# Performance work log

Measured on AMD Instinct MI355X. Metric: run time of the kernel, lower is better.

Reference implementation:

```python
import jax, jax.numpy as jnp
import numpy as np

NUM_PARTS = 10
COP_W = 10.0
COP_K = 100.0
RES = 0.7874


def setup_inputs() -> dict:
    key = jax.random.key(0)
    k1, k2, k3, k4, k5, k6 = jax.random.split(key, 6)
    B, V, F, NHD = 256, 6890, 13776, 20000
    vertices = jax.random.normal(k1, (B, V, 3), dtype=jnp.float32)
    pressure = jax.random.uniform(k2, (B, 120, 40), dtype=jnp.float32)
    bw = jax.random.uniform(k3, (NHD, 3), dtype=jnp.float32)
    bary_w = bw / bw.sum(axis=1, keepdims=True)  # barycentric weights sum to 1
    faces = jax.random.randint(k4, (F, 3), 0, V, dtype=jnp.int64)
    face_sample = jax.random.randint(k5, (NHD,), 0, F, dtype=jnp.int64)
    face_part = jax.random.randint(k6, (F,), 0, NUM_PARTS, dtype=jnp.int64)
    return {"vertices": vertices, "pressure": pressure, "bary_w": bary_w,
            "faces": faces, "face_sample": face_sample, "face_part": face_part}


def cal_cop(pressure, resolution=RES):
    B, Y, X = pressure.shape
    x_coords = jnp.arange(X, dtype=pressure.dtype)
    y_coords = jnp.arange(Y, dtype=pressure.dtype)
    total = pressure.sum(axis=(1, 2))
    total = jnp.where(total == 0, jnp.asarray(1e-8, pressure.dtype), total)
    x_ws = (pressure * x_coords).sum(axis=(1, 2))
    y_ws = (pressure * y_coords[:, None]).sum(axis=(1, 2))
    x_c = x_ws / total
    y_c = y_ws / total
    cop_x = 0.01 * (x_c - 18.0) / resolution
    cop_y = 0.01 * (86.0 - y_c) / resolution
    cop_xy = jnp.stack([cop_x, cop_y, jnp.zeros_like(cop_x)], axis=1)
    cop_sensor_xy = jnp.stack([x_c, y_c], axis=1)
    return cop_xy, cop_sensor_xy


def reference(vertices, pressure, bary_w, faces, face_sample, face_part):
    # ---- per-part volume: signed tetrahedron volume per face, segment-summed per part
    tri = vertices[:, faces]                       # [B, F, 3, 3]
    v0, v1, v2 = tri[:, :, 0], tri[:, :, 1], tri[:, :, 2]
    tet = jnp.einsum('bfi,bfi->bf', v0, jnp.cross(v1, v2)) / 6.0   # [B, F]
    per_part_volume = jax.vmap(
        lambda t: jax.ops.segment_sum(t, face_part, num_segments=NUM_PARTS)
    )(tet)                                          # [B, P]

    # ---- HD mesh: barycentric sampling of 20000 points from faces
    fv = faces[face_sample]                         # [NHD, 3]
    vertices_hd = jnp.einsum('bnkc,nk->bnc', vertices[:, fv], bary_w)  # [B, NHD, 3]

    # ---- vertex-id -> part-volume mapping (one-hot sparse matmul == gather)
    vol_per_vert = per_part_volume[:, face_part[face_sample]]          # [B, NHD]

    com = (vertices_hd * vol_per_vert[..., None]).sum(axis=1) / \
          vol_per_vert.sum(axis=1, keepdims=True)                      # [B, 3]
    com_xy = jnp.stack([com[:, 0], com[:, 1], jnp.zeros_like(com[:, 0])], axis=1)
    com_mat = jnp.stack([com[:, 0] * 48.0, (59.0 / 33.0 - com[:, 1]) * 33.0], axis=1)

    cop_xy, _cop_mat = cal_cop(pressure)

    eps = 1e-6
    vh = vertices_hd[:, :, 1]                       # height above ground plane
    inside = (vh < 0.0).astype(vh.dtype)
    pw = inside * (1.0 - COP_K * vh) + (1.0 - inside) * jnp.exp(-COP_W * vh)
    cop = (vertices_hd * pw[..., None]).sum(axis=1) / (pw.sum(axis=1, keepdims=True) + eps)
    cop_mat_ipman = jnp.stack([cop[:, 0] + 18.0 / 78.74,
                               86.0 / 78.74 - cop[:, 1]], axis=1) * 100.0 * 0.7874

    stability_loss = jnp.linalg.norm(com_xy - cop_xy, axis=1).mean()
    return stability_loss, com_mat, cop_mat_ipman
```

## Files before the change

kernel.cpp:

```cpp
#include <hip/hip_runtime.h>
#include <math.h>

#define NB 256
#define NV 6890
#define NF 13776
#define NFP 16384
#define NHD 20000
#define NHDP 20480
#define NPARTS 10
#define PY 120
#define PX 40
#define THREADS 1024
#define NWAVES (THREADS / 64)

#define WS_DIST_OFF  0
#define WS_TABF_OFF  1024
#define WS_TABS_OFF  (WS_TABF_OFF + NFP * 16)
#define WS_TABW_OFF  (WS_TABS_OFF + NHDP * 16)
#define WS_NEEDED    (WS_TABW_OFF + NHDP * 16)

__device__ __forceinline__ float wred(float v) {
#pragma unroll
    for (int off = 32; off; off >>= 1) v += __shfl_down(v, off, 64);
    return v;
}

__global__ __launch_bounds__(256) void build_tabs(const int* __restrict__ faces,
                                                  const int* __restrict__ face_part,
                                                  const int* __restrict__ face_sample,
                                                  const float* __restrict__ bary_w,
                                                  int4* __restrict__ tabF,
                                                  int4* __restrict__ tabS,
                                                  float4* __restrict__ tabW) {
    const int i = blockIdx.x * 256 + threadIdx.x;
    if (i < NF)
        tabF[i] = make_int4(faces[3 * i + 0], faces[3 * i + 1], faces[3 * i + 2], face_part[i]);
    else if (i < NFP)
        tabF[i] = make_int4(0, 0, 0, 15);
    if (i < NHD) {
        const int fs = face_sample[i];
        tabS[i] = make_int4(faces[3 * fs + 0], faces[3 * fs + 1], faces[3 * fs + 2],
                            face_part[fs]);
        tabW[i] = make_float4(bary_w[3 * i + 0], bary_w[3 * i + 1], bary_w[3 * i + 2], 1.0f);
    } else if (i < NHDP) {
        tabS[i] = make_int4(0, 0, 0, 0);
        tabW[i] = make_float4(0.0f, 0.0f, 0.0f, 0.0f);
    }
}

__device__ __forceinline__ float tet_of(const float2* __restrict__ svxy,
                                        const float* __restrict__ svz, int4 q) {
    const float2 a = svxy[q.x];
    const float2 b = svxy[q.y];
    const float2 c = svxy[q.z];
    const float az = svz[q.x], bz = svz[q.y], cz = svz[q.z];
    return (a.x * (b.y * cz - bz * c.y) + a.y * (bz * c.x - b.x * cz) +
            az * (b.x * c.y - b.y * c.x)) * (1.0f / 6.0f);
}

template <bool TAB>
__global__ __launch_bounds__(THREADS, 4) void stab_main(
    const float* __restrict__ vertices,
    const float* __restrict__ pressure,
    const float* __restrict__ bary_w,
    const int*   __restrict__ faces,
    const int*   __restrict__ face_sample,
    const int*   __restrict__ face_part,
    const int4*  __restrict__ tabF,
    const int4*  __restrict__ tabS,
    const float4* __restrict__ tabW,
    float* __restrict__ out,
    float* __restrict__ dist)
{
    const int b    = blockIdx.x;
    const int tid  = threadIdx.x;
    const int wave = tid >> 6;
    const int lane = tid & 63;

    __shared__ float2 svxy[NV];
    __shared__ float  svz[NV];
    __shared__ float  red[NWAVES][12];
    __shared__ float  ppv[NPARTS];

    const float* vb = vertices + (size_t)b * (NV * 3);
    for (int v = tid; v < NV; v += THREADS) {
        svxy[v] = make_float2(vb[3 * v + 0], vb[3 * v + 1]);
        svz[v]  = vb[3 * v + 2];
    }
    __syncthreads();

    float pv[NPARTS];
#pragma unroll
    for (int p = 0; p < NPARTS; ++p) pv[p] = 0.0f;

    if constexpr (TAB) {
        for (int f0 = tid; f0 < NFP; f0 += 4 * THREADS) {
            const int4 q0 = tabF[f0];
            const int4 q1 = tabF[f0 + THREADS];
            const int4 q2 = tabF[f0 + 2 * THREADS];
            const int4 q3 = tabF[f0 + 3 * THREADS];
            const float t0 = tet_of(svxy, svz, q0);
            const float t1 = tet_of(svxy, svz, q1);
            const float t2 = tet_of(svxy, svz, q2);
            const float t3 = tet_of(svxy, svz, q3);
#pragma unroll
            for (int p = 0; p < NPARTS; ++p) {
                pv[p] += (q0.w == p) ? t0 : 0.0f;
                pv[p] += (q1.w == p) ? t1 : 0.0f;
                pv[p] += (q2.w == p) ? t2 : 0.0f;
                pv[p] += (q3.w == p) ? t3 : 0.0f;
            }
        }
    } else {
        for (int f = tid; f < NF; f += THREADS) {
            const int4 q = make_int4(faces[3 * f + 0], faces[3 * f + 1], faces[3 * f + 2],
                                     face_part[f]);
            const float t = tet_of(svxy, svz, q);
#pragma unroll
            for (int p = 0; p < NPARTS; ++p) pv[p] += (q.w == p) ? t : 0.0f;
        }
    }
#pragma unroll
    for (int p = 0; p < NPARTS; ++p) {
        const float r = wred(pv[p]);
        if (lane == 0) red[wave][p] = r;
    }
    __syncthreads();
    if (tid < NPARTS) {
        float s = 0.0f;
#pragma unroll
        for (int w = 0; w < NWAVES; ++w) s += red[w][tid];
        ppv[tid] = s;
    }
    __syncthreads();

    float cnx = 0.f, cny = 0.f, cd = 0.f;
    float pnx = 0.f, pny = 0.f, pd = 0.f;

    if constexpr (TAB) {
        for (int n0 = tid; n0 < NHDP; n0 += 4 * THREADS) {
            const int4   q0 = tabS[n0];
            const int4   q1 = tabS[n0 + THREADS];
            const int4   q2 = tabS[n0 + 2 * THREADS];
            const int4   q3 = tabS[n0 + 3 * THREADS];
            const float4 w0 = tabW[n0];
            const float4 w1 = tabW[n0 + THREADS];
            const float4 w2 = tabW[n0 + 2 * THREADS];
            const float4 w3 = tabW[n0 + 3 * THREADS];

            const float2 a0 = svxy[q0.x], b0 = svxy[q0.y], c0 = svxy[q0.z];
            const float2 a1 = svxy[q1.x], b1 = svxy[q1.y], c1 = svxy[q1.z];
            const float2 a2 = svxy[q2.x], b2 = svxy[q2.y], c2 = svxy[q2.z];
            const float2 a3 = svxy[q3.x], b3 = svxy[q3.y], c3 = svxy[q3.z];

            const float hx0 = w0.x * a0.x + w0.y * b0.x + w0.z * c0.x;
            const float hy0 = w0.x * a0.y + w0.y * b0.y + w0.z * c0.y;
            const float hx1 = w1.x * a1.x + w1.y * b1.x + w1.z * c1.x;
            const float hy1 = w1.x * a1.y + w1.y * b1.y + w1.z * c1.y;
            const float hx2 = w2.x * a2.x + w2.y * b2.x + w2.z * c2.x;
            const float hy2 = w2.x * a2.y + w2.y * b2.y + w2.z * c2.y;
            const float hx3 = w3.x * a3.x + w3.y * b3.x + w3.z * c3.x;
            const float hy3 = w3.x * a3.y + w3.y * b3.y + w3.z * c3.y;

            const float vol0 = ppv[q0.w] * w0.w;
            const float vol1 = ppv[q1.w] * w1.w;
            const float vol2 = ppv[q2.w] * w2.w;
            const float vol3 = ppv[q3.w] * w3.w;

            const float pw0 = ((hy0 < 0.0f) ? (1.0f - 100.0f * hy0) : __expf(-10.0f * hy0)) * w0.w;
            const float pw1 = ((hy1 < 0.0f) ? (1.0f - 100.0f * hy1) : __expf(-10.0f * hy1)) * w1.w;
            const float pw2 = ((hy2 < 0.0f) ? (1.0f - 100.0f * hy2) : __expf(-10.0f * hy2)) * w2.w;
            const float pw3 = ((hy3 < 0.0f) ? (1.0f - 100.0f * hy3) : __expf(-10.0f * hy3)) * w3.w;

            cnx += hx0 * vol0 + hx1 * vol1 + hx2 * vol2 + hx3 * vol3;
            cny += hy0 * vol0 + hy1 * vol1 + hy2 * vol2 + hy3 * vol3;
            cd  += vol0 + vol1 + vol2 + vol3;
            pnx += hx0 * pw0 + hx1 * pw1 + hx2 * pw2 + hx3 * pw3;
            pny += hy0 * pw0 + hy1 * pw1 + hy2 * pw2 + hy3 * pw3;
            pd  += pw0 + pw1 + pw2 + pw3;
        }
    } else {
        for (int n = tid; n < NHD; n += THREADS) {
            const int fs = face_sample[n];
            const int i0 = faces[3 * fs + 0], i1 = faces[3 * fs + 1], i2 = faces[3 * fs + 2];
            const float w0 = bary_w[3 * n + 0], w1 = bary_w[3 * n + 1], w2 = bary_w[3 * n + 2];
            const float2 a = svxy[i0], bb = svxy[i1], c = svxy[i2];
            const float hx = w0 * a.x + w1 * bb.x + w2 * c.x;
            const float hy = w0 * a.y + w1 * bb.y + w2 * c.y;
            const float vol = ppv[face_part[fs]];
            cnx += hx * vol; cny += hy * vol; cd += vol;
            const float pw = (hy < 0.0f) ? (1.0f - 100.0f * hy) : __expf(-10.0f * hy);
            pnx += hx * pw; pny += hy * pw; pd += pw;
        }
    }

    float pt = 0.f, pxs = 0.f, pys = 0.f;
    const float4* pb4 = (const float4*)(pressure + (size_t)b * (PY * PX));
    for (int i = tid; i < (PY * PX) / 4; i += THREADS) {
        const float4 v = pb4[i];
        const int idx = 4 * i;
        const float xb = (float)(idx % PX);
        const float yb = (float)(idx / PX);
        const float srow = v.x + v.y + v.z + v.w;
        pt  += srow;
        pxs += v.x * xb + v.y * (xb + 1.0f) + v.z * (xb + 2.0f) + v.w * (xb + 3.0f);
        pys += srow * yb;
    }

    float vals[9] = {cnx, cny, cd, pnx, pny, pd, pt, pxs, pys};
#pragma unroll
    for (int k = 0; k < 9; ++k) {
        const float r = wred(vals[k]);
        if (lane == 0) red[wave][k] = r;
    }
    __syncthreads();

    if (tid == 0) {
        float s[9];
#pragma unroll
        for (int k = 0; k < 9; ++k) {
            float acc = 0.0f;
#pragma unroll
            for (int w = 0; w < NWAVES; ++w) acc += red[w][k];
            s[k] = acc;
        }
        const float comx  = s[0] / s[2];
        const float comy  = s[1] / s[2];
        const float copx  = s[3] / (s[5] + 1e-6f);
        const float copy_ = s[4] / (s[5] + 1e-6f);

        out[1 + 2 * b + 0] = comx * 48.0f;
        out[1 + 2 * b + 1] = (59.0f / 33.0f - comy) * 33.0f;
        out[1 + 2 * NB + 2 * b + 0] = (copx + 18.0f / 78.74f) * (100.0f * 0.7874f);
        out[1 + 2 * NB + 2 * b + 1] = (86.0f / 78.74f - copy_) * (100.0f * 0.7874f);

        const float total = (s[6] == 0.0f) ? 1e-8f : s[6];
        const float xc = s[7] / total;
        const float yc = s[8] / total;
        const float pcopx = 0.01f * (xc - 18.0f) / 0.7874f;
        const float pcopy = 0.01f * (86.0f - yc) / 0.7874f;

        const float dx = comx - pcopx;
        const float dy = comy - pcopy;
        dist[b] = sqrtf(dx * dx + dy * dy);
    }
}

__global__ __launch_bounds__(256) void stab_reduce(const float* __restrict__ dist,
                                                   float* __restrict__ out) {
    const int tid = threadIdx.x;
    float v = dist[tid];
    v = wred(v);
    __shared__ float red[4];
    if ((tid & 63) == 0) red[tid >> 6] = v;
    __syncthreads();
    if (tid == 0) out[0] = (red[0] + red[1] + red[2] + red[3]) * (1.0f / 256.0f);
}

extern "C" void kernel_launch(void* const* d_in, const int* in_sizes, int n_in,
                              void* d_out, int out_size, void* d_ws, size_t ws_size,
                              hipStream_t stream) {
    const float* vertices    = (const float*)d_in[0];
    const float* pressure    = (const float*)d_in[1];
    const float* bary_w      = (const float*)d_in[2];
    const int*   faces       = (const int*)d_in[3];
    const int*   face_sample = (const int*)d_in[4];
    const int*   face_part   = (const int*)d_in[5];
    float* out = (float*)d_out;
    char*  ws  = (char*)d_ws;

    float* dist = (float*)(ws + WS_DIST_OFF);

    if (ws_size >= (size_t)WS_NEEDED) {
        int4*   tabF = (int4*)(ws + WS_TABF_OFF);
        int4*   tabS = (int4*)(ws + WS_TABS_OFF);
        float4* tabW = (float4*)(ws + WS_TABW_OFF);
        build_tabs<<<(NHDP + 255) / 256, 256, 0, stream>>>(faces, face_part, face_sample,
                                                           bary_w, tabF, tabS, tabW);
        stab_main<true><<<NB, THREADS, 0, stream>>>(vertices, pressure, bary_w, faces,
                                                    face_sample, face_part, tabF, tabS, tabW,
                                                    out, dist);
    } else {
        stab_main<false><<<NB, THREADS, 0, stream>>>(vertices, pressure, bary_w, faces,
                                                     face_sample, face_part, nullptr, nullptr,
                                                     nullptr, out, dist);
    }
    stab_reduce<<<1, 256, 0, stream>>>(dist, out);
}
```

Measured before the change: 33.21 us.

## Split fused per-batch kernel into volume pass and two-block HD sampling pass

The single per-batch kernel is split in two. One kernel computes part volumes and pressure sums. A second kernel handles the HD-point weighted sums using two blocks per batch element, with a smaller shared footprint (xy only) that allows more blocks per CU. A finishing kernel combines the partials and computes the loss. This adds a kernel launch and a second reload of the vertices in exchange for more parallelism and occupancy, and it drops the no-workspace fallback path.

```diff
diff --git a/kernel.cpp b/kernel.cpp
--- a/kernel.cpp
+++ b/kernel.cpp
@@ -10,11 +10,10 @@
 #define NPARTS 10
 #define PY 120
 #define PX 40
-#define THREADS 1024
-#define NWAVES (THREADS / 64)
-
-#define WS_DIST_OFF  0
-#define WS_TABF_OFF  1024
+
+#define WS_ACC_OFF   0
+#define WS_PB_OFF    16384
+#define WS_TABF_OFF  32768
 #define WS_TABS_OFF  (WS_TABF_OFF + NFP * 16)
 #define WS_TABW_OFF  (WS_TABS_OFF + NHDP * 16)
 #define WS_NEEDED    (WS_TABW_OFF + NHDP * 16)
@@ -58,20 +57,10 @@
             az * (b.x * c.y - b.y * c.x)) * (1.0f / 6.0f);
 }
 
-template <bool TAB>
-__global__ __launch_bounds__(THREADS, 4) void stab_main(
-    const float* __restrict__ vertices,
-    const float* __restrict__ pressure,
-    const float* __restrict__ bary_w,
-    const int*   __restrict__ faces,
-    const int*   __restrict__ face_sample,
-    const int*   __restrict__ face_part,
-    const int4*  __restrict__ tabF,
-    const int4*  __restrict__ tabS,
-    const float4* __restrict__ tabW,
-    float* __restrict__ out,
-    float* __restrict__ dist)
-{
+__global__ __launch_bounds__(1024, 4) void kA(const float* __restrict__ vertices,
+                                              const float* __restrict__ pressure,
+                                              const int4* __restrict__ tabF,
+                                              float* __restrict__ acc) {
     const int b    = blockIdx.x;
     const int tid  = threadIdx.x;
     const int wave = tid >> 6;
@@ -79,11 +68,10 @@
 
     __shared__ float2 svxy[NV];
     __shared__ float  svz[NV];
-    __shared__ float  red[NWAVES][12];
-    __shared__ float  ppv[NPARTS];
+    __shared__ float  red[16][13];
 
     const float* vb = vertices + (size_t)b * (NV * 3);
-    for (int v = tid; v < NV; v += THREADS) {
+    for (int v = tid; v < NV; v += 1024) {
         svxy[v] = make_float2(vb[3 * v + 0], vb[3 * v + 1]);
         svz[v]  = vb[3 * v + 2];
     }
@@ -93,110 +81,27 @@
 #pragma unroll
     for (int p = 0; p < NPARTS; ++p) pv[p] = 0.0f;
 
-    if constexpr (TAB) {
-        for (int f0 = tid; f0 < NFP; f0 += 4 * THREADS) {
-            const int4 q0 = tabF[f0];
-            const int4 q1 = tabF[f0 + THREADS];
-            const int4 q2 = tabF[f0 + 2 * THREADS];
-            const int4 q3 = tabF[f0 + 3 * THREADS];
-            const float t0 = tet_of(svxy, svz, q0);
-            const float t1 = tet_of(svxy, svz, q1);
-            const float t2 = tet_of(svxy, svz, q2);
-            const float t3 = tet_of(svxy, svz, q3);
-#pragma unroll
-            for (int p = 0; p < NPARTS; ++p) {
-                pv[p] += (q0.w == p) ? t0 : 0.0f;
-                pv[p] += (q1.w == p) ? t1 : 0.0f;
-                pv[p] += (q2.w == p) ? t2 : 0.0f;
-                pv[p] += (q3.w == p) ? t3 : 0.0f;
-            }
-        }
-    } else {
-        for (int f = tid; f < NF; f += THREADS) {
-            const int4 q = make_int4(faces[3 * f + 0], faces[3 * f + 1], faces[3 * f + 2],
-                                     face_part[f]);
-            const float t = tet_of(svxy, svz, q);
-#pragma unroll
-            for (int p = 0; p < NPARTS; ++p) pv[p] += (q.w == p) ? t : 0.0f;
-        }
-    }
-#pragma unroll
-    for (int p = 0; p < NPARTS; ++p) {
-        const float r = wred(pv[p]);
-        if (lane == 0) red[wave][p] = r;
-    }
-    __syncthreads();
-    if (tid < NPARTS) {
-        float s = 0.0f;
-#pragma unroll
-        for (int w = 0; w < NWAVES; ++w) s += red[w][tid];
-        ppv[tid] = s;
-    }
-    __syncthreads();
-
-    float cnx = 0.f, cny = 0.f, cd = 0.f;
-    float pnx = 0.f, pny = 0.f, pd = 0.f;
-
-    if constexpr (TAB) {
-        for (int n0 = tid; n0 < NHDP; n0 += 4 * THREADS) {
-            const int4   q0 = tabS[n0];
-            const int4   q1 = tabS[n0 + THREADS];
-            const int4   q2 = tabS[n0 + 2 * THREADS];
-            const int4   q3 = tabS[n0 + 3 * THREADS];
-            const float4 w0 = tabW[n0];
-            const float4 w1 = tabW[n0 + THREADS];
-            const float4 w2 = tabW[n0 + 2 * THREADS];
-            const float4 w3 = tabW[n0 + 3 * THREADS];
-
-            const float2 a0 = svxy[q0.x], b0 = svxy[q0.y], c0 = svxy[q0.z];
-            const float2 a1 = svxy[q1.x], b1 = svxy[q1.y], c1 = svxy[q1.z];
-            const float2 a2 = svxy[q2.x], b2 = svxy[q2.y], c2 = svxy[q2.z];
-            const float2 a3 = svxy[q3.x], b3 = svxy[q3.y], c3 = svxy[q3.z];
-
-            const float hx0 = w0.x * a0.x + w0.y * b0.x + w0.z * c0.x;
-            const float hy0 = w0.x * a0.y + w0.y * b0.y + w0.z * c0.y;
-            const float hx1 = w1.x * a1.x + w1.y * b1.x + w1.z * c1.x;
-            const float hy1 = w1.x * a1.y + w1.y * b1.y + w1.z * c1.y;
-            const float hx2 = w2.x * a2.x + w2.y * b2.x + w2.z * c2.x;
-            const float hy2 = w2.x * a2.y + w2.y * b2.y + w2.z * c2.y;
-            const float hx3 = w3.x * a3.x + w3.y * b3.x + w3.z * c3.x;
-            const float hy3 = w3.x * a3.y + w3.y * b3.y + w3.z * c3.y;
-
-            const float vol0 = ppv[q0.w] * w0.w;
-            const float vol1 = ppv[q1.w] * w1.w;
-            const float vol2 = ppv[q2.w] * w2.w;
-            const float vol3 = ppv[q3.w] * w3.w;
-
-            const float pw0 = ((hy0 < 0.0f) ? (1.0f - 100.0f * hy0) : __expf(-10.0f * hy0)) * w0.w;
-            const float pw1 = ((hy1 < 0.0f) ? (1.0f - 100.0f * hy1) : __expf(-10.0f * hy1)) * w1.w;
-            const float pw2 = ((hy2 < 0.0f) ? (1.0f - 100.0f * hy2) : __expf(-10.0f * hy2)) * w2.w;
-            const float pw3 = ((hy3 < 0.0f) ? (1.0f - 100.0f * hy3) : __expf(-10.0f * hy3)) * w3.w;
-
-            cnx += hx0 * vol0 + hx1 * vol1 + hx2 * vol2 + hx3 * vol3;
-            cny += hy0 * vol0 + hy1 * vol1 + hy2 * vol2 + hy3 * vol3;
-            cd  += vol0 + vol1 + vol2 + vol3;
-            pnx += hx0 * pw0 + hx1 * pw1 + hx2 * pw2 + hx3 * pw3;
-            pny += hy0 * pw0 + hy1 * pw1 + hy2 * pw2 + hy3 * pw3;
-            pd  += pw0 + pw1 + pw2 + pw3;
-        }
-    } else {
-        for (int n = tid; n < NHD; n += THREADS) {
-            const int fs = face_sample[n];
-            const int i0 = faces[3 * fs + 0], i1 = faces[3 * fs + 1], i2 = faces[3 * fs + 2];
-            const float w0 = bary_w[3 * n + 0], w1 = bary_w[3 * n + 1], w2 = bary_w[3 * n + 2];
-            const float2 a = svxy[i0], bb = svxy[i1], c = svxy[i2];
-            const float hx = w0 * a.x + w1 * bb.x + w2 * c.x;
-            const float hy = w0 * a.y + w1 * bb.y + w2 * c.y;
-            const float vol = ppv[face_part[fs]];
-            cnx += hx * vol; cny += hy * vol; cd += vol;
-            const float pw = (hy < 0.0f) ? (1.0f - 100.0f * hy) : __expf(-10.0f * hy);
-            pnx += hx * pw; pny += hy * pw; pd += pw;
+    for (int f0 = tid; f0 < NFP; f0 += 4096) {
+        const int4 q0 = tabF[f0];
+        const int4 q1 = tabF[f0 + 1024];
+        const int4 q2 = tabF[f0 + 2048];
+        const int4 q3 = tabF[f0 + 3072];
+        const float t0 = tet_of(svxy, svz, q0);
+        const float t1 = tet_of(svxy, svz, q1);
+        const float t2 = tet_of(svxy, svz, q2);
+        const float t3 = tet_of(svxy, svz, q3);
+#pragma unroll
+        for (int p = 0; p < NPARTS; ++p) {
+            pv[p] += (q0.w == p) ? t0 : 0.0f;
+            pv[p] += (q1.w == p) ? t1 : 0.0f;
+            pv[p] += (q2.w == p) ? t2 : 0.0f;
+            pv[p] += (q3.w == p) ? t3 : 0.0f;
         }
     }
 
     float pt = 0.f, pxs = 0.f, pys = 0.f;
     const float4* pb4 = (const float4*)(pressure + (size_t)b * (PY * PX));
-    for (int i = tid; i < (PY * PX) / 4; i += THREADS) {
+    for (int i = tid; i < (PY * PX) / 4; i += 1024) {
         const float4 v = pb4[i];
         const int idx = 4 * i;
         const float xb = (float)(idx % PX);
@@ -207,54 +112,134 @@
         pys += srow * yb;
     }
 
-    float vals[9] = {cnx, cny, cd, pnx, pny, pd, pt, pxs, pys};
-#pragma unroll
-    for (int k = 0; k < 9; ++k) {
+    float vals[13] = {pv[0], pv[1], pv[2], pv[3], pv[4], pv[5], pv[6], pv[7], pv[8], pv[9],
+                      pt, pxs, pys};
+#pragma unroll
+    for (int k = 0; k < 13; ++k) {
         const float r = wred(vals[k]);
         if (lane == 0) red[wave][k] = r;
     }
     __syncthreads();
-
-    if (tid == 0) {
-        float s[9];
-#pragma unroll
-        for (int k = 0; k < 9; ++k) {
-            float acc = 0.0f;
-#pragma unroll
-            for (int w = 0; w < NWAVES; ++w) acc += red[w][k];
-            s[k] = acc;
-        }
-        const float comx  = s[0] / s[2];
-        const float comy  = s[1] / s[2];
-        const float copx  = s[3] / (s[5] + 1e-6f);
-        const float copy_ = s[4] / (s[5] + 1e-6f);
-
-        out[1 + 2 * b + 0] = comx * 48.0f;
-        out[1 + 2 * b + 1] = (59.0f / 33.0f - comy) * 33.0f;
-        out[1 + 2 * NB + 2 * b + 0] = (copx + 18.0f / 78.74f) * (100.0f * 0.7874f);
-        out[1 + 2 * NB + 2 * b + 1] = (86.0f / 78.74f - copy_) * (100.0f * 0.7874f);
-
-        const float total = (s[6] == 0.0f) ? 1e-8f : s[6];
-        const float xc = s[7] / total;
-        const float yc = s[8] / total;
-        const float pcopx = 0.01f * (xc - 18.0f) / 0.7874f;
-        const float pcopy = 0.01f * (86.0f - yc) / 0.7874f;
-
-        const float dx = comx - pcopx;
-        const float dy = comy - pcopy;
-        dist[b] = sqrtf(dx * dx + dy * dy);
-    }
-}
-
-__global__ __launch_bounds__(256) void stab_reduce(const float* __restrict__ dist,
+    if (tid < 13) {
+        float s = 0.0f;
+#pragma unroll
+        for (int w = 0; w < 16; ++w) s += red[w][tid];
+        acc[b * 16 + tid] = s;
+    }
+}
+
+__global__ __launch_bounds__(1024, 8) void kB(const float* __restrict__ vertices,
+                                              const int4*  __restrict__ tabS,
+                                              const float4* __restrict__ tabW,
+                                              const float* __restrict__ acc,
+                                              float* __restrict__ pB) {
+    const int bid  = blockIdx.x;
+    const int b    = bid >> 1;
+    const int half = bid & 1;
+    const int tid  = threadIdx.x;
+    const int wave = tid >> 6;
+    const int lane = tid & 63;
+
+    __shared__ float2 svxy[NV];
+    __shared__ float  red[16][6];
+    __shared__ float  ppv[NPARTS];
+
+    const float* vb = vertices + (size_t)b * (NV * 3);
+    for (int v = tid; v < NV; v += 1024)
+        svxy[v] = make_float2(vb[3 * v + 0], vb[3 * v + 1]);
+    if (tid < NPARTS) ppv[tid] = acc[b * 16 + tid];
+    __syncthreads();
+
+    float cnx = 0.f, cny = 0.f, cd = 0.f;
+    float pnx = 0.f, pny = 0.f, pd = 0.f;
+    const float KEXP = -14.426950408889634f;
+
+    const int nbase = half * (NHDP / 2);
+    for (int n0 = nbase + tid; n0 < nbase + NHDP / 2; n0 += 2048) {
+        const int4   q0 = tabS[n0];
+        const int4   q1 = tabS[n0 + 1024];
+        const float4 w0 = tabW[n0];
+        const float4 w1 = tabW[n0 + 1024];
+
+        const float2 a0 = svxy[q0.x], b0 = svxy[q0.y], c0 = svxy[q0.z];
+        const float2 a1 = svxy[q1.x], b1 = svxy[q1.y], c1 = svxy[q1.z];
+
+        const float hx0 = w0.x * a0.x + w0.y * b0.x + w0.z * c0.x;
+        const float hy0 = w0.x * a0.y + w0.y * b0.y + w0.z * c0.y;
+        const float hx1 = w1.x * a1.x + w1.y * b1.x + w1.z * c1.x;
+        const float hy1 = w1.x * a1.y + w1.y * b1.y + w1.z * c1.y;
+
+        const float vol0 = ppv[q0.w] * w0.w;
+        const float vol1 = ppv[q1.w] * w1.w;
+
+        const float pw0 = ((hy0 < 0.0f) ? (1.0f - 100.0f * hy0) : exp2f(KEXP * hy0)) * w0.w;
+        const float pw1 = ((hy1 < 0.0f) ? (1.0f - 100.0f * hy1) : exp2f(KEXP * hy1)) * w1.w;
+
+        cnx += hx0 * vol0 + hx1 * vol1;
+        cny += hy0 * vol0 + hy1 * vol1;
+        cd  += vol0 + vol1;
+        pnx += hx0 * pw0 + hx1 * pw1;
+        pny += hy0 * pw0 + hy1 * pw1;
+        pd  += pw0 + pw1;
+    }
+
+    float vals[6] = {cnx, cny, cd, pnx, pny, pd};
+#pragma unroll
+    for (int k = 0; k < 6; ++k) {
+        const float r = wred(vals[k]);
+        if (lane == 0) red[wave][k] = r;
+    }
+    __syncthreads();
+    if (tid < 6) {
+        float s = 0.0f;
+#pragma unroll
+        for (int w = 0; w < 16; ++w) s += red[w][tid];
+        pB[tid * 512 + bid] = s;
+    }
+}
+
+__global__ __launch_bounds__(256) void stab_finish(const float* __restrict__ acc,
+                                                   const float* __restrict__ pB,
                                                    float* __restrict__ out) {
-    const int tid = threadIdx.x;
-    float v = dist[tid];
+    const int b    = threadIdx.x;
+    const int wave = b >> 6;
+    const int lane = b & 63;
+    __shared__ float red[4];
+
+    const float cnx = pB[0 * 512 + 2 * b] + pB[0 * 512 + 2 * b + 1];
+    const float cny = pB[1 * 512 + 2 * b] + pB[1 * 512 + 2 * b + 1];
+    const float cd  = pB[2 * 512 + 2 * b] + pB[2 * 512 + 2 * b + 1];
+    const float pnx = pB[3 * 512 + 2 * b] + pB[3 * 512 + 2 * b + 1];
+    const float pny = pB[4 * 512 + 2 * b] + pB[4 * 512 + 2 * b + 1];
+    const float pd  = pB[5 * 512 + 2 * b] + pB[5 * 512 + 2 * b + 1];
+    const float pt  = acc[b * 16 + 10];
+    const float pxs = acc[b * 16 + 11];
+    const float pys = acc[b * 16 + 12];
+
+    const float comx  = cnx / cd;
+    const float comy  = cny / cd;
+    const float copx  = pnx / (pd + 1e-6f);
+    const float copy_ = pny / (pd + 1e-6f);
+
+    out[1 + 2 * b + 0] = comx * 48.0f;
+    out[1 + 2 * b + 1] = (59.0f / 33.0f - comy) * 33.0f;
+    out[1 + 2 * NB + 2 * b + 0] = (copx + 18.0f / 78.74f) * (100.0f * 0.7874f);
+    out[1 + 2 * NB + 2 * b + 1] = (86.0f / 78.74f - copy_) * (100.0f * 0.7874f);
+
+    const float total = (pt == 0.0f) ? 1e-8f : pt;
+    const float xc = pxs / total;
+    const float yc = pys / total;
+    const float pcopx = 0.01f * (xc - 18.0f) / 0.7874f;
+    const float pcopy = 0.01f * (86.0f - yc) / 0.7874f;
+
+    const float dx = comx - pcopx;
+    const float dy = comy - pcopy;
+    float v = sqrtf(dx * dx + dy * dy);
+
     v = wred(v);
-    __shared__ float red[4];
-    if ((tid & 63) == 0) red[tid >> 6] = v;
-    __syncthreads();
-    if (tid == 0) out[0] = (red[0] + red[1] + red[2] + red[3]) * (1.0f / 256.0f);
+    if (lane == 0) red[wave] = v;
+    __syncthreads();
+    if (b == 0) out[0] = (red[0] + red[1] + red[2] + red[3]) * (1.0f / NB);
 }
 
 extern "C" void kernel_launch(void* const* d_in, const int* in_sizes, int n_in,
@@ -269,21 +254,15 @@
     float* out = (float*)d_out;
     char*  ws  = (char*)d_ws;
 
-    float* dist = (float*)(ws + WS_DIST_OFF);
-
-    if (ws_size >= (size_t)WS_NEEDED) {
-        int4*   tabF = (int4*)(ws + WS_TABF_OFF);
-        int4*   tabS = (int4*)(ws + WS_TABS_OFF);
-        float4* tabW = (float4*)(ws + WS_TABW_OFF);
-        build_tabs<<<(NHDP + 255) / 256, 256, 0, stream>>>(faces, face_part, face_sample,
-                                                           bary_w, tabF, tabS, tabW);
-        stab_main<true><<<NB, THREADS, 0, stream>>>(vertices, pressure, bary_w, faces,
-                                                    face_sample, face_part, tabF, tabS, tabW,
-                                                    out, dist);
-    } else {
-        stab_main<false><<<NB, THREADS, 0, stream>>>(vertices, pressure, bary_w, faces,
-                                                     face_sample, face_part, nullptr, nullptr,
-                                                     nullptr, out, dist);
-    }
-    stab_reduce<<<1, 256, 0, stream>>>(dist, out);
-}
+    float*  acc  = (float*)(ws + WS_ACC_OFF);
+    float*  pB   = (float*)(ws + WS_PB_OFF);
+    int4*   tabF = (int4*)(ws + WS_TABF_OFF);
+    int4*   tabS = (int4*)(ws + WS_TABS_OFF);
+    float4* tabW = (float4*)(ws + WS_TABW_OFF);
+
+    build_tabs<<<(NHDP + 255) / 256, 256, 0, stream>>>(faces, face_part, face_sample,
+                                                       bary_w, tabF, tabS, tabW);
+    kA<<<NB, 1024, 0, stream>>>(vertices, pressure, tabF, acc);
+    kB<<<NB * 2, 1024, 0, stream>>>(vertices, tabS, tabW, acc, pB);
+    stab_finish<<<1, 256, 0, stream>>>(acc, pB, out);
+}
```

After: 42.33 us. 27.5% more time.
